# Optimization experiments

Measured on AMD Instinct MI355X. Metric: run time of the kernel, lower is better.

The kernel has to match this reference:

```python
import jax, jax.numpy as jnp
import numpy as np

N_NODES = 100000
N_EDGES = 1250000
HID = 64          # structure_hidden_dim
N_RBF = 32
N_GRAPHS = 512
N_EXPERTS = 8
N_LAYERS = 3
CUTOFF = 6.0
MAX_Z = 100
GATE_IN = HID + N_EXPERTS  # 72
G1, G2 = 64, 32            # gate_hidden_dims


def setup_inputs() -> dict:
    key = jax.random.key(0)
    ks = jax.random.split(key, 32)
    s = 0.05
    inp = {
        'z': jax.random.randint(ks[0], (N_NODES,), 0, MAX_Z),
        'edge_index': jax.random.randint(ks[1], (2, N_EDGES), 0, N_NODES),
        'edge_weight': jax.random.uniform(ks[2], (N_EDGES,), dtype=jnp.float32) * CUTOFF,
        'batch': jnp.sort(jax.random.randint(ks[3], (N_NODES,), 0, N_GRAPHS)),
        'mlip_energies': jax.random.normal(ks[4], (N_GRAPHS, N_EXPERTS), dtype=jnp.float32),
        # SchNet parameters (torch nn.Linear convention: W is [out, in])
        'emb': jax.random.normal(ks[5], (MAX_Z, HID)) * s,
        'fW1': jax.random.normal(ks[6], (N_LAYERS, HID, N_RBF)) * s,
        'fb1': jnp.zeros((N_LAYERS, HID)),
        'fW2': jax.random.normal(ks[7], (N_LAYERS, HID, HID)) * s,
        'fb2': jnp.zeros((N_LAYERS, HID)),
        'dW': jax.random.normal(ks[8], (N_LAYERS, HID, HID)) * s,
        'db': jnp.zeros((N_LAYERS, HID)),
        'uW1': jax.random.normal(ks[9], (N_LAYERS, HID, HID)) * s,
        'ub1': jnp.zeros((N_LAYERS, HID)),
        'uW2': jax.random.normal(ks[10], (N_LAYERS, HID, HID)) * s,
        'ub2': jnp.zeros((N_LAYERS, HID)),
        # Gating MLP: (HID+E) -> 64 -> 32 -> E
        'gW1': jax.random.normal(ks[11], (G1, GATE_IN)) * s,
        'gb1': jnp.zeros((G1,)),
        'gW2': jax.random.normal(ks[12], (G2, G1)) * s,
        'gb2': jnp.zeros((G2,)),
        'gW3': jax.random.normal(ks[13], (N_EXPERTS, G2)) * s,
        'gb3': jnp.zeros((N_EXPERTS,)),
    }
    return inp


def reference(z, edge_index, edge_weight, batch, mlip_energies,
              emb, fW1, fb1, fW2, fb2, dW, db, uW1, ub1, uW2, ub2,
              gW1, gb1, gW2, gb2, gW3, gb3):
    src, dst = edge_index[0], edge_index[1]

    # Gaussian smearing of distances -> [E, N_RBF]
    offsets = jnp.linspace(0.0, CUTOFF, N_RBF, dtype=edge_weight.dtype)
    delta = offsets[1] - offsets[0]
    coeff = -0.5 / (delta * delta)
    diff = edge_weight[:, None] - offsets
    edge_attr = jnp.exp(coeff * diff * diff)

    # atom embedding [N, HID]
    x = emb[z]

    for i in range(N_LAYERS):
        # filter network: Linear -> SiLU -> Linear on RBF features [E, HID]
        f = jax.nn.silu(edge_attr @ fW1[i].T + fb1[i]) @ fW2[i].T + fb2[i]
        # gather + dense + elementwise filter -> messages [E, HID]
        msg = (x[src] @ dW[i].T + db[i]) * f
        # scatter-add to destination nodes [N, HID]
        agg = jax.ops.segment_sum(msg, dst, num_segments=N_NODES)
        # residual update MLP
        x = x + (jax.nn.silu(agg @ uW1[i].T + ub1[i]) @ uW2[i].T + ub2[i])

    # mean pool per graph [G, HID]
    pooled = jax.ops.segment_sum(x, batch, num_segments=N_GRAPHS)
    counts = jax.ops.segment_sum(jnp.ones((N_NODES,), x.dtype), batch, num_segments=N_GRAPHS)
    structure_embedding = pooled / jnp.maximum(counts, 1.0)[:, None]

    # gated MoE head
    gate_in = jnp.concatenate([structure_embedding, mlip_energies], axis=-1)
    h = jax.nn.relu(gate_in @ gW1.T + gb1)
    h = jax.nn.relu(h @ gW2.T + gb2)
    logits = h @ gW3.T + gb3
    weights = jax.nn.softmax(logits, axis=-1)
    prediction = jnp.sum(mlip_energies * weights, axis=-1)
    return (logits, weights, prediction)
```

## Files before the change

kernel.cpp:

```cpp
#include <hip/hip_runtime.h>
#include <hip/hip_fp16.h>
#include <math.h>

#define N_NODES   100000
#define N_EDGES   1250000
#define HID       64
#define N_RBF     32
#define N_GRAPHS  512
#define N_EXPERTS 8
#define N_LAYERS  3
#define CUTOFF    6.0f
#define GATE_IN   72
#define G1_DIM    64
#define G2_DIM    32
#define K_TAB     4096
#define N_BUCKET  391
#define BUCKET_CAP 4608
#define CHUNK_A   8192

typedef short short8 __attribute__((ext_vector_type(8)));
typedef float float4v __attribute__((ext_vector_type(4)));

__device__ __forceinline__ unsigned enc8(float v) {
  unsigned short u = __half_as_ushort(__float2half(v));
  return (unsigned)((unsigned short)(u + 0x80u) >> 8);
}
__device__ __forceinline__ float dec8(unsigned b) {
  return __half2float(__ushort_as_half((unsigned short)(b << 8)));
}
__device__ __forceinline__ unsigned short bf16(float f) {
  unsigned u = __float_as_uint(f);
  u += 0x7fffu + ((u >> 16) & 1u);
  return (unsigned short)(u >> 16);
}

__global__ __launch_bounds__(256) void build_tab(
    const float* __restrict__ fW1, const float* __restrict__ fb1,
    const float* __restrict__ fW2, const float* __restrict__ fb2,
    float* __restrict__ tab) {
  __shared__ float W1s[64][33];
  __shared__ float W2s[64][65];
  __shared__ float rbfs[4][32];
  __shared__ float h1s[4][64];
  int t = threadIdx.x;
  int wv = t >> 6, lane = t & 63;
  int layer = blockIdx.x / 1025;
  int k = (blockIdx.x % 1025) * 4 + wv;

  for (int i = t; i < 64 * 32; i += 256) W1s[i >> 5][i & 31] = fW1[layer * 2048 + i];
  for (int i = t; i < 64 * 64; i += 256) W2s[i >> 6][i & 63] = fW2[layer * 4096 + i];

  float w = (CUTOFF / (float)K_TAB) * (float)k;
  const float delta = CUTOFF / (float)(N_RBF - 1);
  const float coeff = -0.5f / (delta * delta);
  __syncthreads();

  if (lane < N_RBF) {
    float d = w - delta * (float)lane;
    rbfs[wv][lane] = expf(coeff * d * d);
  }
  __syncthreads();

  float s = fb1[layer * HID + lane];
#pragma unroll
  for (int j = 0; j < N_RBF; j++) s += rbfs[wv][j] * W1s[lane][j];
  h1s[wv][lane] = s / (1.0f + expf(-s));
  __syncthreads();

  float f = fb2[layer * HID + lane];
#pragma unroll
  for (int c = 0; c < HID; c++) f += h1s[wv][c] * W2s[lane][c];
  if (k <= K_TAB) tab[(layer * (K_TAB + 1) + k) * HID + lane] = f;
}

__global__ __launch_bounds__(256) void pack_tab8(
    const float* __restrict__ tab, unsigned short* __restrict__ tabP8) {
  int i = blockIdx.x * 256 + threadIdx.x;
  if (i >= N_LAYERS * K_TAB * 64) return;
  int layer = i / (K_TAB * 64);
  int r = i - layer * (K_TAB * 64);
  const float* base = tab + layer * (K_TAB + 1) * 64;
  tabP8[i] = (unsigned short)(enc8(base[r]) | (enc8(base[r + 64]) << 8));
}

__global__ __launch_bounds__(256) void conv_w(
    const float* __restrict__ dW, const float* __restrict__ uW1,
    const float* __restrict__ uW2, unsigned short* __restrict__ dWh,
    unsigned short* __restrict__ uW1h, unsigned short* __restrict__ uW2h) {
  int i = blockIdx.x * 256 + threadIdx.x;
  if (i < N_LAYERS * 4096) {
    dWh[i]  = bf16(dW[i]);
    uW1h[i] = bf16(uW1[i]);
    uW2h[i] = bf16(uW2[i]);
  }
}

__global__ __launch_bounds__(256) void embed_kernel(
    const int* __restrict__ z, const float* __restrict__ emb,
    float* __restrict__ x) {
  int i = blockIdx.x * 256 + threadIdx.x;
  if (i < N_NODES * HID) {
    int n = i >> 6, h = i & 63;
    x[i] = emb[z[n] * HID + h];
  }
}

__global__ __launch_bounds__(256) void partitionA(
    const int* __restrict__ src, const int* __restrict__ dst,
    const float* __restrict__ ew, int* __restrict__ gcnt,
    uint2* __restrict__ stage) {
  __shared__ int hist[N_BUCKET];
  __shared__ int base[N_BUCKET];
  int t = threadIdx.x;
  int e0 = blockIdx.x * CHUNK_A;
  int e1 = e0 + CHUNK_A; if (e1 > N_EDGES) e1 = N_EDGES;

  for (int i = t; i < N_BUCKET; i += 256) hist[i] = 0;
  __syncthreads();
  for (int e = e0 + t; e < e1; e += 256)
    atomicAdd(&hist[dst[e] >> 8], 1);
  __syncthreads();
  for (int i = t; i < N_BUCKET; i += 256) {
    int c = hist[i];
    base[i] = c ? atomicAdd(&gcnt[i], c) : 0;
    hist[i] = 0;
  }
  __syncthreads();
  for (int e = e0 + t; e < e1; e += 256) {
    int d = dst[e];
    int b = d >> 8;
    int r = base[b] + atomicAdd(&hist[b], 1);
    if (r < BUCKET_CAP) {
      float uq = ew[e] * ((float)K_TAB * 8.0f / CUTOFF);
      int wq = (int)(uq + 0.5f);
      if (wq > 32767) wq = 32767;
      stage[(size_t)b * BUCKET_CAP + r] =
          make_uint2(((unsigned)src[e] << 15) | (unsigned)wq, (unsigned)d);
    }
  }
}

__global__ __launch_bounds__(512) void bscan_kernel(
    const int* __restrict__ gcnt, int* __restrict__ bbase,
    int* __restrict__ rowstart) {
  __shared__ int sh[512];
  int t = threadIdx.x;
  int v = 0;
  if (t < N_BUCKET) {
    v = gcnt[t];
    if (v > BUCKET_CAP) v = BUCKET_CAP;
  }
  sh[t] = v;
  __syncthreads();
  for (int off = 1; off < 512; off <<= 1) {
    int add = (t >= off) ? sh[t - off] : 0;
    __syncthreads();
    sh[t] += add;
    __syncthreads();
  }
  if (t < N_BUCKET) bbase[t] = sh[t] - v;
  if (t == N_BUCKET - 1) {
    bbase[N_BUCKET] = sh[t];
    rowstart[N_NODES] = sh[t];
  }
}

__global__ __launch_bounds__(256) void sortB(
    const int* __restrict__ bbase, const uint2* __restrict__ stage,
    int* __restrict__ rowstart, unsigned* __restrict__ recs) {
  __shared__ int cnt[256];
  __shared__ int scn[256];
  __shared__ unsigned dest[BUCKET_CAP];
  int t = threadIdx.x;
  int b = blockIdx.x;
  int node0 = b << 8;
  int base = bbase[b];
  int total = bbase[b + 1] - base;
  const uint2* st = stage + (size_t)b * BUCKET_CAP;

  cnt[t] = 0;
  __syncthreads();
  for (int k = t; k < total; k += 256) atomicAdd(&cnt[(int)st[k].y - node0], 1);
  __syncthreads();
  int v = cnt[t];
  scn[t] = v;
  __syncthreads();
  for (int off = 1; off < 256; off <<= 1) {
    int add = (t >= off) ? scn[t - off] : 0;
    __syncthreads();
    scn[t] += add;
    __syncthreads();
  }
  int excl = scn[t] - v;
  int n = node0 + t;
  if (n < N_NODES) rowstart[n] = base + excl;
  scn[t] = excl;
  cnt[t] = 0;
  __syncthreads();
  for (int k = t; k < total; k += 256) {
    uint2 e = st[k];
    int ln = (int)e.y - node0;
    int r = atomicAdd(&cnt[ln], 1);
    dest[scn[ln] + r] = e.x;
  }
  __syncthreads();
  for (int k = t; k < total; k += 256) recs[base + k] = dest[k];
}

__global__ __launch_bounds__(256, 4) void dense64(
    const float* __restrict__ x, const unsigned short* __restrict__ Wh,
    const float* __restrict__ b, unsigned char* __restrict__ yb) {
  __shared__ __align__(16) unsigned char smem[18432];
  short* As = (short*)smem;
  short* Bs = As + 64 * 72;
  float* Es = (float*)smem;
  int t = threadIdx.x;
  int row0 = blockIdx.x * 64;

#pragma unroll
  for (int it = 0; it < 4; it++) {
    int i = it * 1024 + t * 4;
    int r = i >> 6, c = i & 63;
    int gr = row0 + r;
    float4 v = make_float4(0.f, 0.f, 0.f, 0.f);
    if (gr < N_NODES) v = *(const float4*)&x[(size_t)gr * 64 + c];
    short4 h;
    h.x = (short)bf16(v.x); h.y = (short)bf16(v.y);
    h.z = (short)bf16(v.z); h.w = (short)bf16(v.w);
    *(short4*)&As[r * 72 + c] = h;
  }
#pragma unroll
  for (int it = 0; it < 2; it++) {
    int i = it * 2048 + t * 8;
    int r = i >> 6, c = i & 63;
    *(uint4*)&Bs[r * 72 + c] = *(const uint4*)&Wh[i];
  }
  __syncthreads();

  int lane = t & 63, wv = t >> 6;
  int m = lane & 15, quad = lane >> 4;
  const short* arow = As + (wv * 16 + m) * 72 + quad * 8;
  short8 a0 = *(const short8*)arow;
  short8 a1 = *(const short8*)(arow + 32);
  float4v acc[4];
#pragma unroll
  for (int ct = 0; ct < 4; ct++) {
    const short* brow = Bs + (ct * 16 + m) * 72 + quad * 8;
    short8 bf0 = *(const short8*)brow;
    short8 bf1 = *(const short8*)(brow + 32);
    float bj = b[ct * 16 + m];
    float4v c = {bj, bj, bj, bj};
    c = __builtin_amdgcn_mfma_f32_16x16x32_bf16(a0, bf0, c, 0, 0, 0);
    c = __builtin_amdgcn_mfma_f32_16x16x32_bf16(a1, bf1, c, 0, 0, 0);
    acc[ct] = c;
  }
  __syncthreads();
#pragma unroll
  for (int ct = 0; ct < 4; ct++)
#pragma unroll
    for (int r = 0; r < 4; r++)
      Es[(wv * 16 + quad * 4 + r) * 68 + ct * 16 + m] = acc[ct][r];
  __syncthreads();
  {
    int row = t >> 2, c0 = (t & 3) * 16;
    int gr = row0 + row;
    if (gr < N_NODES) {
      unsigned w[4];
#pragma unroll
      for (int q = 0; q < 4; q++) {
        const float* p = &Es[row * 68 + c0 + 4 * q];
        w[q] = enc8(p[0]) | (enc8(p[1]) << 8) | (enc8(p[2]) << 16) | (enc8(p[3]) << 24);
      }
      *(uint4*)&yb[(size_t)gr * 64 + c0] = make_uint4(w[0], w[1], w[2], w[3]);
    }
  }
}

__global__ __launch_bounds__(256, 4) void update64(
    const unsigned short* __restrict__ aggb,
    const unsigned short* __restrict__ W1h, const float* __restrict__ b1,
    const unsigned short* __restrict__ W2h, const float* __restrict__ b2,
    float* __restrict__ x) {
  __shared__ __align__(16) unsigned char smem[18432];
  short* As = (short*)smem;
  short* Bs = As + 64 * 72;
  float* Es = (float*)smem;
  int t = threadIdx.x;
  int row0 = blockIdx.x * 64;
  int lane = t & 63, wv = t >> 6;
  int m = lane & 15, quad = lane >> 4;

#pragma unroll
  for (int it = 0; it < 2; it++) {
    int i = it * 2048 + t * 8;
    int r = i >> 6, c = i & 63;
    int gr = row0 + r;
    uint4 v = make_uint4(0u, 0u, 0u, 0u);
    if (gr < N_NODES) v = *(const uint4*)&aggb[(size_t)gr * 64 + c];
    *(uint4*)&As[r * 72 + c] = v;
    *(uint4*)&Bs[r * 72 + c] = *(const uint4*)&W1h[i];
  }
  __syncthreads();

  const short* arow = As + (wv * 16 + m) * 72 + quad * 8;
  float4v acc[4];
  {
    short8 a0 = *(const short8*)arow;
    short8 a1 = *(const short8*)(arow + 32);
#pragma unroll
    for (int ct = 0; ct < 4; ct++) {
      const short* brow = Bs + (ct * 16 + m) * 72 + quad * 8;
      short8 bf0 = *(const short8*)brow;
      short8 bf1 = *(const short8*)(brow + 32);
      float bj = b1[ct * 16 + m];
      float4v c = {bj, bj, bj, bj};
      c = __builtin_amdgcn_mfma_f32_16x16x32_bf16(a0, bf0, c, 0, 0, 0);
      c = __builtin_amdgcn_mfma_f32_16x16x32_bf16(a1, bf1, c, 0, 0, 0);
      acc[ct] = c;
    }
  }
  __syncthreads();
#pragma unroll
  for (int ct = 0; ct < 4; ct++)
#pragma unroll
    for (int r = 0; r < 4; r++) {
      float s = acc[ct][r];
      float h = s / (1.0f + expf(-s));
      As[(wv * 16 + quad * 4 + r) * 72 + ct * 16 + m] = (short)bf16(h);
    }
#pragma unroll
  for (int it = 0; it < 2; it++) {
    int i = it * 2048 + t * 8;
    int r = i >> 6, c = i & 63;
    *(uint4*)&Bs[r * 72 + c] = *(const uint4*)&W2h[i];
  }
  __syncthreads();

  {
    short8 a0 = *(const short8*)arow;
    short8 a1 = *(const short8*)(arow + 32);
#pragma unroll
    for (int ct = 0; ct < 4; ct++) {
      const short* brow = Bs + (ct * 16 + m) * 72 + quad * 8;
      short8 bf0 = *(const short8*)brow;
      short8 bf1 = *(const short8*)(brow + 32);
      float bj = b2[ct * 16 + m];
      float4v c = {bj, bj, bj, bj};
      c = __builtin_amdgcn_mfma_f32_16x16x32_bf16(a0, bf0, c, 0, 0, 0);
      c = __builtin_amdgcn_mfma_f32_16x16x32_bf16(a1, bf1, c, 0, 0, 0);
      acc[ct] = c;
    }
  }
  __syncthreads();
#pragma unroll
  for (int ct = 0; ct < 4; ct++)
#pragma unroll
    for (int r = 0; r < 4; r++)
      Es[(wv * 16 + quad * 4 + r) * 68 + ct * 16 + m] = acc[ct][r];
  __syncthreads();
  {
    int row = t >> 2, c0 = (t & 3) * 16;
    int gr = row0 + row;
    if (gr < N_NODES) {
      float* xp = x + (size_t)gr * 64 + c0;
#pragma unroll
      for (int q = 0; q < 4; q++) {
        float4 xv = *(float4*)(xp + 4 * q);
        float4 av = *(const float4*)&Es[row * 68 + c0 + 4 * q];
        xv.x += av.x; xv.y += av.y; xv.z += av.z; xv.w += av.w;
        *(float4*)(xp + 4 * q) = xv;
      }
    }
  }
}

__global__ __launch_bounds__(256) void gather_kernel(
    const int* __restrict__ rowstart, const unsigned* __restrict__ recs,
    const unsigned short* __restrict__ tabP8,
    const unsigned char* __restrict__ yb,
    unsigned short* __restrict__ aggb) {
  int d = blockIdx.x * 4 + (threadIdx.x >> 6);
  int lane = threadIdx.x & 63;
  int b0 = __builtin_amdgcn_readfirstlane(rowstart[d]);
  int b1 = __builtin_amdgcn_readfirstlane(rowstart[d + 1]);
  float acc = 0.0f;
  int j = b0;
  for (; j + 4 <= b1; j += 4) {
    unsigned u0 = recs[j];
    unsigned u1 = recs[j + 1];
    unsigned u2 = recs[j + 2];
    unsigned u3 = recs[j + 3];
    unsigned y0 = yb[((u0 >> 15) << 6) + lane];
    unsigned y1 = yb[((u1 >> 15) << 6) + lane];
    unsigned y2 = yb[((u2 >> 15) << 6) + lane];
    unsigned y3 = yb[((u3 >> 15) << 6) + lane];
    unsigned p0 = tabP8[(((u0 & 32767u) >> 3) << 6) + lane];
    unsigned p1 = tabP8[(((u1 & 32767u) >> 3) << 6) + lane];
    unsigned p2 = tabP8[(((u2 & 32767u) >> 3) << 6) + lane];
    unsigned p3 = tabP8[(((u3 & 32767u) >> 3) << 6) + lane];
    float fr0 = (float)(u0 & 7u) * 0.125f;
    float fr1 = (float)(u1 & 7u) * 0.125f;
    float fr2 = (float)(u2 & 7u) * 0.125f;
    float fr3 = (float)(u3 & 7u) * 0.125f;
    float a0 = dec8(p0 & 0xffu), g0 = dec8(p0 >> 8);
    float a1 = dec8(p1 & 0xffu), g1 = dec8(p1 >> 8);
    float a2 = dec8(p2 & 0xffu), g2 = dec8(p2 >> 8);
    float a3 = dec8(p3 & 0xffu), g3 = dec8(p3 >> 8);
    acc += dec8(y0) * (a0 + (g0 - a0) * fr0);
    acc += dec8(y1) * (a1 + (g1 - a1) * fr1);
    acc += dec8(y2) * (a2 + (g2 - a2) * fr2);
    acc += dec8(y3) * (a3 + (g3 - a3) * fr3);
  }
  for (; j < b1; j++) {
    unsigned u = recs[j];
    unsigned yv = yb[((u >> 15) << 6) + lane];
    unsigned p = tabP8[(((u & 32767u) >> 3) << 6) + lane];
    float fr = (float)(u & 7u) * 0.125f;
    float a = dec8(p & 0xffu), g = dec8(p >> 8);
    acc += dec8(yv) * (a + (g - a) * fr);
  }
  aggb[(size_t)d * 64 + lane] = bf16(acc);
}

__global__ __launch_bounds__(256) void pool_kernel(
    const float* __restrict__ x, const int* __restrict__ batch,
    float* __restrict__ pooled, float* __restrict__ counts) {
  int wid = (blockIdx.x * 256 + threadIdx.x) >> 6;
  int lane = threadIdx.x & 63;
  int n0 = wid * 64;
  if (n0 >= N_NODES) return;
  int n1 = n0 + 64; if (n1 > N_NODES) n1 = N_NODES;
  int curg = batch[n0];
  float acc = 0.0f, cnt = 0.0f;
  for (int n = n0; n < n1; n++) {
    int g = batch[n];
    if (g != curg) {
      unsafeAtomicAdd(&pooled[curg * 64 + lane], acc);
      if (lane == 0) unsafeAtomicAdd(&counts[curg], cnt);
      curg = g; acc = 0.0f; cnt = 0.0f;
    }
    acc += x[n * 64 + lane];
    cnt += 1.0f;
  }
  unsafeAtomicAdd(&pooled[curg * 64 + lane], acc);
  if (lane == 0) unsafeAtomicAdd(&counts[curg], cnt);
}

__global__ __launch_bounds__(256) void gate_kernel(
    const float* __restrict__ pooled, const float* __restrict__ counts,
    const float* __restrict__ mlip,
    const float* __restrict__ gW1, const float* __restrict__ gb1,
    const float* __restrict__ gW2, const float* __restrict__ gb2,
    const float* __restrict__ gW3, const float* __restrict__ gb3,
    float* __restrict__ out) {
  __shared__ float ins[4][GATE_IN];
  __shared__ float h1s[4][G1_DIM];
  __shared__ float h2s[4][G2_DIM];
  __shared__ float lg[4][N_EXPERTS];
  int wv = threadIdx.x >> 6, lane = threadIdx.x & 63;
  int g = blockIdx.x * 4 + wv;

  float cnt = counts[g];
  if (cnt < 1.0f) cnt = 1.0f;
  ins[wv][lane] = pooled[g * 64 + lane] / cnt;
  if (lane < N_EXPERTS) ins[wv][64 + lane] = mlip[g * N_EXPERTS + lane];
  __syncthreads();

  {
    float s = gb1[lane];
    for (int c = 0; c < GATE_IN; c++) s += ins[wv][c] * gW1[lane * GATE_IN + c];
    h1s[wv][lane] = fmaxf(s, 0.0f);
  }
  __syncthreads();
  if (lane < G2_DIM) {
    float s = gb2[lane];
    for (int c = 0; c < G1_DIM; c++) s += h1s[wv][c] * gW2[lane * G1_DIM + c];
    h2s[wv][lane] = fmaxf(s, 0.0f);
  }
  __syncthreads();
  if (lane < N_EXPERTS) {
    float s = gb3[lane];
    for (int c = 0; c < G2_DIM; c++) s += h2s[wv][c] * gW3[lane * G2_DIM + c];
    lg[wv][lane] = s;
  }
  __syncthreads();
  if (lane < N_EXPERTS) {
    float m = -1e30f;
    for (int j = 0; j < N_EXPERTS; j++) m = fmaxf(m, lg[wv][j]);
    float den = 0.0f;
    for (int j = 0; j < N_EXPERTS; j++) den += expf(lg[wv][j] - m);
    float wgt = expf(lg[wv][lane] - m) / den;
    out[g * 8 + lane] = lg[wv][lane];
    out[N_GRAPHS * 8 + g * 8 + lane] = wgt;
    if (lane == 0) {
      float p = 0.0f;
      for (int j = 0; j < N_EXPERTS; j++)
        p += mlip[g * 8 + j] * expf(lg[wv][j] - m) / den;
      out[N_GRAPHS * 16 + g] = p;
    }
  }
}

extern "C" void kernel_launch(void* const* d_in, const int* in_sizes, int n_in,
                              void* d_out, int out_size, void* d_ws, size_t ws_size,
                              hipStream_t stream) {
  const int*   z     = (const int*)  d_in[0];
  const int*   ei    = (const int*)  d_in[1];
  const float* ew    = (const float*)d_in[2];
  const int*   batch = (const int*)  d_in[3];
  const float* mlip  = (const float*)d_in[4];
  const float* emb   = (const float*)d_in[5];
  const float* fW1   = (const float*)d_in[6];
  const float* fb1   = (const float*)d_in[7];
  const float* fW2   = (const float*)d_in[8];
  const float* fb2   = (const float*)d_in[9];
  const float* dW    = (const float*)d_in[10];
  const float* db    = (const float*)d_in[11];
  const float* uW1   = (const float*)d_in[12];
  const float* ub1   = (const float*)d_in[13];
  const float* uW2   = (const float*)d_in[14];
  const float* ub2   = (const float*)d_in[15];
  const float* gW1   = (const float*)d_in[16];
  const float* gb1   = (const float*)d_in[17];
  const float* gW2   = (const float*)d_in[18];
  const float* gb2   = (const float*)d_in[19];
  const float* gW3   = (const float*)d_in[20];
  const float* gb3   = (const float*)d_in[21];

  const int* src = ei;
  const int* dst = ei + N_EDGES;

  float* ws = (float*)d_ws;
  float*          x        = ws;
  unsigned char*  yb       = (unsigned char*)(ws + 6400000);
  unsigned short* aggb     = (unsigned short*)(ws + 8000000);
  float*          tab      = ws + 11200000;
  unsigned short* tabP8    = (unsigned short*)(ws + 11986624);
  float*          pooled   = ws + 12379840;
  float*          counts   = ws + 12412608;
  int*            rowstart = (int*)(ws + 12413120);
  unsigned*       recs     = (unsigned*)(ws + 12513121);
  int*            gcnt     = (int*)(ws + 13763121);
  int*            bbase    = (int*)(ws + 13763512);
  uint2*          stage    = (uint2*)(ws + 13763904);
  unsigned short* dWh      = (unsigned short*)(ws + 17367360);
  unsigned short* uW1h     = dWh + N_LAYERS * 4096;
  unsigned short* uW2h     = uW1h + N_LAYERS * 4096;

  hipMemsetAsync(gcnt, 0, N_BUCKET * sizeof(int), stream);
  partitionA<<<(N_EDGES + CHUNK_A - 1) / CHUNK_A, 256, 0, stream>>>(
      src, dst, ew, gcnt, stage);
  bscan_kernel<<<1, 512, 0, stream>>>(gcnt, bbase, rowstart);
  sortB<<<N_BUCKET, 256, 0, stream>>>(bbase, stage, rowstart, recs);

  build_tab<<<N_LAYERS * 1025, 256, 0, stream>>>(fW1, fb1, fW2, fb2, tab);
  pack_tab8<<<(N_LAYERS * K_TAB * 64) / 256, 256, 0, stream>>>(tab, tabP8);
  conv_w<<<(N_LAYERS * 4096 + 255) / 256, 256, 0, stream>>>(dW, uW1, uW2, dWh, uW1h, uW2h);
  embed_kernel<<<(N_NODES * HID + 255) / 256, 256, 0, stream>>>(z, emb, x);

  for (int i = 0; i < N_LAYERS; i++) {
    dense64<<<(N_NODES + 63) / 64, 256, 0, stream>>>(x, dWh + i * 4096, db + i * 64, yb);
    gather_kernel<<<(N_NODES + 3) / 4, 256, 0, stream>>>(
        rowstart, recs, tabP8 + i * K_TAB * 64, yb, aggb);
    update64<<<(N_NODES + 63) / 64, 256, 0, stream>>>(aggb, uW1h + i * 4096, ub1 + i * 64,
                                                      uW2h + i * 4096, ub2 + i * 64, x);
  }

  hipMemsetAsync(pooled, 0, (size_t)(N_GRAPHS * HID + N_GRAPHS) * sizeof(float), stream);
  pool_kernel<<<(N_NODES / 64 + 1 + 3) / 4, 256, 0, stream>>>(x, batch, pooled, counts);
  gate_kernel<<<N_GRAPHS / 4, 256, 0, stream>>>(pooled, counts, mlip,
                                                gW1, gb1, gW2, gb2, gW3, gb3,
                                                (float*)d_out);
}
```

Before: 419.4 us.

## Fuse update with next-layer dense, drop embed kernel, single-byte filter table

The residual update kernel now also runs the next layer's dense projection and writes the quantized messages. The first layer reads embeddings straight from z/emb, so the separate embed kernel and a full read-modify-write of x go away. The filter table becomes one byte per entry, taken as the midpoint of adjacent bins instead of an interpolated pair, which halves table traffic in the gather and removes the interpolation arithmetic but loses accuracy. The change also shrinks the partition chunk size and gives the sort kernel 512 threads.

```diff
diff --git a/kernel.cpp b/kernel.cpp
--- a/kernel.cpp
+++ b/kernel.cpp
@@ -16,7 +16,7 @@
 #define K_TAB     4096
 #define N_BUCKET  391
 #define BUCKET_CAP 4608
-#define CHUNK_A   8192
+#define CHUNK_A   2048
 
 typedef short short8 __attribute__((ext_vector_type(8)));
 typedef float float4v __attribute__((ext_vector_type(4)));
@@ -74,13 +74,13 @@
 }
 
 __global__ __launch_bounds__(256) void pack_tab8(
-    const float* __restrict__ tab, unsigned short* __restrict__ tabP8) {
+    const float* __restrict__ tab, unsigned char* __restrict__ tab8) {
   int i = blockIdx.x * 256 + threadIdx.x;
   if (i >= N_LAYERS * K_TAB * 64) return;
   int layer = i / (K_TAB * 64);
   int r = i - layer * (K_TAB * 64);
   const float* base = tab + layer * (K_TAB + 1) * 64;
-  tabP8[i] = (unsigned short)(enc8(base[r]) | (enc8(base[r + 64]) << 8));
+  tab8[i] = (unsigned char)enc8(0.5f * (base[r] + base[r + 64]));
 }
 
 __global__ __launch_bounds__(256) void conv_w(
@@ -95,16 +95,6 @@
   }
 }
 
-__global__ __launch_bounds__(256) void embed_kernel(
-    const int* __restrict__ z, const float* __restrict__ emb,
-    float* __restrict__ x) {
-  int i = blockIdx.x * 256 + threadIdx.x;
-  if (i < N_NODES * HID) {
-    int n = i >> 6, h = i & 63;
-    x[i] = emb[z[n] * HID + h];
-  }
-}
-
 __global__ __launch_bounds__(256) void partitionA(
     const int* __restrict__ src, const int* __restrict__ dst,
     const float* __restrict__ ew, int* __restrict__ gcnt,
@@ -131,11 +121,11 @@
     int b = d >> 8;
     int r = base[b] + atomicAdd(&hist[b], 1);
     if (r < BUCKET_CAP) {
-      float uq = ew[e] * ((float)K_TAB * 8.0f / CUTOFF);
-      int wq = (int)(uq + 0.5f);
-      if (wq > 32767) wq = 32767;
+      float uq = ew[e] * ((float)K_TAB / CUTOFF);
+      int wq = (int)uq;
+      if (wq > K_TAB - 1) wq = K_TAB - 1;
       stage[(size_t)b * BUCKET_CAP + r] =
-          make_uint2(((unsigned)src[e] << 15) | (unsigned)wq, (unsigned)d);
+          make_uint2(((unsigned)src[e] << 12) | (unsigned)wq, (unsigned)d);
     }
   }
 }
@@ -165,7 +155,7 @@
   }
 }
 
-__global__ __launch_bounds__(256) void sortB(
+__global__ __launch_bounds__(512) void sortB(
     const int* __restrict__ bbase, const uint2* __restrict__ stage,
     int* __restrict__ rowstart, unsigned* __restrict__ recs) {
   __shared__ int cnt[256];
@@ -178,37 +168,40 @@
   int total = bbase[b + 1] - base;
   const uint2* st = stage + (size_t)b * BUCKET_CAP;
 
-  cnt[t] = 0;
-  __syncthreads();
-  for (int k = t; k < total; k += 256) atomicAdd(&cnt[(int)st[k].y - node0], 1);
-  __syncthreads();
-  int v = cnt[t];
-  scn[t] = v;
+  if (t < 256) cnt[t] = 0;
+  __syncthreads();
+  for (int k = t; k < total; k += 512) atomicAdd(&cnt[(int)st[k].y - node0], 1);
+  __syncthreads();
+  int v = 0;
+  if (t < 256) { v = cnt[t]; scn[t] = v; }
   __syncthreads();
   for (int off = 1; off < 256; off <<= 1) {
-    int add = (t >= off) ? scn[t - off] : 0;
+    int add = (t < 256 && t >= off) ? scn[t - off] : 0;
     __syncthreads();
-    scn[t] += add;
+    if (t < 256) scn[t] += add;
     __syncthreads();
   }
-  int excl = scn[t] - v;
-  int n = node0 + t;
-  if (n < N_NODES) rowstart[n] = base + excl;
-  scn[t] = excl;
-  cnt[t] = 0;
-  __syncthreads();
-  for (int k = t; k < total; k += 256) {
+  if (t < 256) {
+    int excl = scn[t] - v;
+    int n = node0 + t;
+    if (n < N_NODES) rowstart[n] = base + excl;
+    scn[t] = excl;
+    cnt[t] = 0;
+  }
+  __syncthreads();
+  for (int k = t; k < total; k += 512) {
     uint2 e = st[k];
     int ln = (int)e.y - node0;
     int r = atomicAdd(&cnt[ln], 1);
     dest[scn[ln] + r] = e.x;
   }
   __syncthreads();
-  for (int k = t; k < total; k += 256) recs[base + k] = dest[k];
-}
-
-__global__ __launch_bounds__(256, 4) void dense64(
-    const float* __restrict__ x, const unsigned short* __restrict__ Wh,
+  for (int k = t; k < total; k += 512) recs[base + k] = dest[k];
+}
+
+__global__ __launch_bounds__(256, 4) void dense0(
+    const int* __restrict__ z, const float* __restrict__ emb,
+    const unsigned short* __restrict__ Wh,
     const float* __restrict__ b, unsigned char* __restrict__ yb) {
   __shared__ __align__(16) unsigned char smem[18432];
   short* As = (short*)smem;
@@ -223,7 +216,10 @@
     int r = i >> 6, c = i & 63;
     int gr = row0 + r;
     float4 v = make_float4(0.f, 0.f, 0.f, 0.f);
-    if (gr < N_NODES) v = *(const float4*)&x[(size_t)gr * 64 + c];
+    if (gr < N_NODES) {
+      int zi = z[gr];
+      v = *(const float4*)&emb[(size_t)zi * 64 + c];
+    }
     short4 h;
     h.x = (short)bf16(v.x); h.y = (short)bf16(v.y);
     h.z = (short)bf16(v.z); h.w = (short)bf16(v.w);
@@ -276,20 +272,38 @@
   }
 }
 
-__global__ __launch_bounds__(256, 4) void update64(
+__global__ __launch_bounds__(256, 4) void update_dense(
     const unsigned short* __restrict__ aggb,
-    const unsigned short* __restrict__ W1h, const float* __restrict__ b1,
-    const unsigned short* __restrict__ W2h, const float* __restrict__ b2,
-    float* __restrict__ x) {
-  __shared__ __align__(16) unsigned char smem[18432];
-  short* As = (short*)smem;
-  short* Bs = As + 64 * 72;
-  float* Es = (float*)smem;
+    const unsigned short* __restrict__ W1h, const float* __restrict__ ub1,
+    const unsigned short* __restrict__ W2h, const float* __restrict__ ub2,
+    float* __restrict__ x,
+    const int* __restrict__ z, const float* __restrict__ emb,
+    const unsigned short* __restrict__ dWn, const float* __restrict__ dbn,
+    unsigned char* __restrict__ yb) {
+  __shared__ __align__(16) short A1[64 * 72];
+  __shared__ __align__(16) short B1[64 * 72];
+  __shared__ __align__(16) float E[64 * 68];
   int t = threadIdx.x;
   int row0 = blockIdx.x * 64;
   int lane = t & 63, wv = t >> 6;
   int m = lane & 15, quad = lane >> 4;
 
+#pragma unroll
+  for (int it = 0; it < 4; it++) {
+    int i = it * 1024 + t * 4;
+    int r = i >> 6, c = i & 63;
+    int gr = row0 + r;
+    float4 v = make_float4(0.f, 0.f, 0.f, 0.f);
+    if (gr < N_NODES) {
+      if (z) {
+        int zi = z[gr];
+        v = *(const float4*)&emb[(size_t)zi * 64 + c];
+      } else {
+        v = *(const float4*)&x[(size_t)gr * 64 + c];
+      }
+    }
+    *(float4*)&E[r * 68 + c] = v;
+  }
 #pragma unroll
   for (int it = 0; it < 2; it++) {
     int i = it * 2048 + t * 8;
@@ -297,22 +311,22 @@
     int gr = row0 + r;
     uint4 v = make_uint4(0u, 0u, 0u, 0u);
     if (gr < N_NODES) v = *(const uint4*)&aggb[(size_t)gr * 64 + c];
-    *(uint4*)&As[r * 72 + c] = v;
-    *(uint4*)&Bs[r * 72 + c] = *(const uint4*)&W1h[i];
-  }
-  __syncthreads();
-
-  const short* arow = As + (wv * 16 + m) * 72 + quad * 8;
+    *(uint4*)&A1[r * 72 + c] = v;
+    *(uint4*)&B1[r * 72 + c] = *(const uint4*)&W1h[i];
+  }
+  __syncthreads();
+
+  const short* arow = A1 + (wv * 16 + m) * 72 + quad * 8;
   float4v acc[4];
   {
     short8 a0 = *(const short8*)arow;
     short8 a1 = *(const short8*)(arow + 32);
 #pragma unroll
     for (int ct = 0; ct < 4; ct++) {
-      const short* brow = Bs + (ct * 16 + m) * 72 + quad * 8;
+      const short* brow = B1 + (ct * 16 + m) * 72 + quad * 8;
       short8 bf0 = *(const short8*)brow;
       short8 bf1 = *(const short8*)(brow + 32);
-      float bj = b1[ct * 16 + m];
+      float bj = ub1[ct * 16 + m];
       float4v c = {bj, bj, bj, bj};
       c = __builtin_amdgcn_mfma_f32_16x16x32_bf16(a0, bf0, c, 0, 0, 0);
       c = __builtin_amdgcn_mfma_f32_16x16x32_bf16(a1, bf1, c, 0, 0, 0);
@@ -326,13 +340,13 @@
     for (int r = 0; r < 4; r++) {
       float s = acc[ct][r];
       float h = s / (1.0f + expf(-s));
-      As[(wv * 16 + quad * 4 + r) * 72 + ct * 16 + m] = (short)bf16(h);
+      A1[(wv * 16 + quad * 4 + r) * 72 + ct * 16 + m] = (short)bf16(h);
     }
 #pragma unroll
   for (int it = 0; it < 2; it++) {
     int i = it * 2048 + t * 8;
     int r = i >> 6, c = i & 63;
-    *(uint4*)&Bs[r * 72 + c] = *(const uint4*)&W2h[i];
+    *(uint4*)&B1[r * 72 + c] = *(const uint4*)&W2h[i];
   }
   __syncthreads();
 
@@ -341,10 +355,10 @@
     short8 a1 = *(const short8*)(arow + 32);
 #pragma unroll
     for (int ct = 0; ct < 4; ct++) {
-      const short* brow = Bs + (ct * 16 + m) * 72 + quad * 8;
+      const short* brow = B1 + (ct * 16 + m) * 72 + quad * 8;
       short8 bf0 = *(const short8*)brow;
       short8 bf1 = *(const short8*)(brow + 32);
-      float bj = b2[ct * 16 + m];
+      float bj = ub2[ct * 16 + m];
       float4v c = {bj, bj, bj, bj};
       c = __builtin_amdgcn_mfma_f32_16x16x32_bf16(a0, bf0, c, 0, 0, 0);
       c = __builtin_amdgcn_mfma_f32_16x16x32_bf16(a1, bf1, c, 0, 0, 0);
@@ -356,7 +370,7 @@
   for (int ct = 0; ct < 4; ct++)
 #pragma unroll
     for (int r = 0; r < 4; r++)
-      Es[(wv * 16 + quad * 4 + r) * 68 + ct * 16 + m] = acc[ct][r];
+      E[(wv * 16 + quad * 4 + r) * 68 + ct * 16 + m] += acc[ct][r];
   __syncthreads();
   {
     int row = t >> 2, c0 = (t & 3) * 16;
@@ -364,19 +378,69 @@
     if (gr < N_NODES) {
       float* xp = x + (size_t)gr * 64 + c0;
 #pragma unroll
+      for (int q = 0; q < 4; q++)
+        *(float4*)(xp + 4 * q) = *(const float4*)&E[row * 68 + c0 + 4 * q];
+    }
+  }
+  if (!dWn) return;
+
+#pragma unroll
+  for (int it = 0; it < 4; it++) {
+    int i = it * 1024 + t * 4;
+    int r = i >> 6, c = i & 63;
+    float4 v = *(const float4*)&E[r * 68 + c];
+    short4 h;
+    h.x = (short)bf16(v.x); h.y = (short)bf16(v.y);
+    h.z = (short)bf16(v.z); h.w = (short)bf16(v.w);
+    *(short4*)&A1[r * 72 + c] = h;
+  }
+#pragma unroll
+  for (int it = 0; it < 2; it++) {
+    int i = it * 2048 + t * 8;
+    int r = i >> 6, c = i & 63;
+    *(uint4*)&B1[r * 72 + c] = *(const uint4*)&dWn[i];
+  }
+  __syncthreads();
+  {
+    short8 a0 = *(const short8*)arow;
+    short8 a1 = *(const short8*)(arow + 32);
+#pragma unroll
+    for (int ct = 0; ct < 4; ct++) {
+      const short* brow = B1 + (ct * 16 + m) * 72 + quad * 8;
+      short8 bf0 = *(const short8*)brow;
+      short8 bf1 = *(const short8*)(brow + 32);
+      float bj = dbn[ct * 16 + m];
+      float4v c = {bj, bj, bj, bj};
+      c = __builtin_amdgcn_mfma_f32_16x16x32_bf16(a0, bf0, c, 0, 0, 0);
+      c = __builtin_amdgcn_mfma_f32_16x16x32_bf16(a1, bf1, c, 0, 0, 0);
+      acc[ct] = c;
+    }
+  }
+  __syncthreads();
+#pragma unroll
+  for (int ct = 0; ct < 4; ct++)
+#pragma unroll
+    for (int r = 0; r < 4; r++)
+      E[(wv * 16 + quad * 4 + r) * 68 + ct * 16 + m] = acc[ct][r];
+  __syncthreads();
+  {
+    int row = t >> 2, c0 = (t & 3) * 16;
+    int gr = row0 + row;
+    if (gr < N_NODES) {
+      unsigned w[4];
+#pragma unroll
       for (int q = 0; q < 4; q++) {
-        float4 xv = *(float4*)(xp + 4 * q);
-        float4 av = *(const float4*)&Es[row * 68 + c0 + 4 * q];
-        xv.x += av.x; xv.y += av.y; xv.z += av.z; xv.w += av.w;
-        *(float4*)(xp + 4 * q) = xv;
+        const float* p = &E[row * 68 + c0 + 4 * q];
+        w[q] = enc8(p[0]) | (enc8(p[1]) << 8) | (enc8(p[2]) << 16) | (enc8(p[3]) << 24);
       }
+      *(uint4*)&yb[(size_t)gr * 64 + c0] = make_uint4(w[0], w[1], w[2], w[3]);
     }
   }
 }
 
 __global__ __launch_bounds__(256) void gather_kernel(
     const int* __restrict__ rowstart, const unsigned* __restrict__ recs,
-    const unsigned short* __restrict__ tabP8,
+    const unsigned char* __restrict__ tab8,
     const unsigned char* __restrict__ yb,
     unsigned short* __restrict__ aggb) {
   int d = blockIdx.x * 4 + (threadIdx.x >> 6);
@@ -390,34 +454,24 @@
     unsigned u1 = recs[j + 1];
     unsigned u2 = recs[j + 2];
     unsigned u3 = recs[j + 3];
-    unsigned y0 = yb[((u0 >> 15) << 6) + lane];
-    unsigned y1 = yb[((u1 >> 15) << 6) + lane];
-    unsigned y2 = yb[((u2 >> 15) << 6) + lane];
-    unsigned y3 = yb[((u3 >> 15) << 6) + lane];
-    unsigned p0 = tabP8[(((u0 & 32767u) >> 3) << 6) + lane];
-    unsigned p1 = tabP8[(((u1 & 32767u) >> 3) << 6) + lane];
-    unsigned p2 = tabP8[(((u2 & 32767u) >> 3) << 6) + lane];
-    unsigned p3 = tabP8[(((u3 & 32767u) >> 3) << 6) + lane];
-    float fr0 = (float)(u0 & 7u) * 0.125f;
-    float fr1 = (float)(u1 & 7u) * 0.125f;
-    float fr2 = (float)(u2 & 7u) * 0.125f;
-    float fr3 = (float)(u3 & 7u) * 0.125f;
-    float a0 = dec8(p0 & 0xffu), g0 = dec8(p0 >> 8);
-    float a1 = dec8(p1 & 0xffu), g1 = dec8(p1 >> 8);
-    float a2 = dec8(p2 & 0xffu), g2 = dec8(p2 >> 8);
-    float a3 = dec8(p3 & 0xffu), g3 = dec8(p3 >> 8);
-    acc += dec8(y0) * (a0 + (g0 - a0) * fr0);
-    acc += dec8(y1) * (a1 + (g1 - a1) * fr1);
-    acc += dec8(y2) * (a2 + (g2 - a2) * fr2);
-    acc += dec8(y3) * (a3 + (g3 - a3) * fr3);
+    unsigned y0 = yb[((u0 >> 12) << 6) + lane];
+    unsigned y1 = yb[((u1 >> 12) << 6) + lane];
+    unsigned y2 = yb[((u2 >> 12) << 6) + lane];
+    unsigned y3 = yb[((u3 >> 12) << 6) + lane];
+    unsigned f0 = tab8[((u0 & 4095u) << 6) + lane];
+    unsigned f1 = tab8[((u1 & 4095u) << 6) + lane];
+    unsigned f2 = tab8[((u2 & 4095u) << 6) + lane];
+    unsigned f3 = tab8[((u3 & 4095u) << 6) + lane];
+    acc += dec8(y0) * dec8(f0);
+    acc += dec8(y1) * dec8(f1);
+    acc += dec8(y2) * dec8(f2);
+    acc += dec8(y3) * dec8(f3);
   }
   for (; j < b1; j++) {
     unsigned u = recs[j];
-    unsigned yv = yb[((u >> 15) << 6) + lane];
-    unsigned p = tabP8[(((u & 32767u) >> 3) << 6) + lane];
-    float fr = (float)(u & 7u) * 0.125f;
-    float a = dec8(p & 0xffu), g = dec8(p >> 8);
-    acc += dec8(yv) * (a + (g - a) * fr);
+    unsigned yv = yb[((u >> 12) << 6) + lane];
+    unsigned fv = tab8[((u & 4095u) << 6) + lane];
+    acc += dec8(yv) * dec8(fv);
   }
   aggb[(size_t)d * 64 + lane] = bf16(acc);
 }
@@ -535,15 +589,15 @@
   unsigned char*  yb       = (unsigned char*)(ws + 6400000);
   unsigned short* aggb     = (unsigned short*)(ws + 8000000);
   float*          tab      = ws + 11200000;
-  unsigned short* tabP8    = (unsigned short*)(ws + 11986624);
-  float*          pooled   = ws + 12379840;
-  float*          counts   = ws + 12412608;
-  int*            rowstart = (int*)(ws + 12413120);
-  unsigned*       recs     = (unsigned*)(ws + 12513121);
-  int*            gcnt     = (int*)(ws + 13763121);
-  int*            bbase    = (int*)(ws + 13763512);
-  uint2*          stage    = (uint2*)(ws + 13763904);
-  unsigned short* dWh      = (unsigned short*)(ws + 17367360);
+  unsigned char*  tab8     = (unsigned char*)(ws + 11986624);
+  float*          pooled   = ws + 12183232;
+  float*          counts   = ws + 12216000;
+  int*            rowstart = (int*)(ws + 12216512);
+  unsigned*       recs     = (unsigned*)(ws + 12316513);
+  int*            gcnt     = (int*)(ws + 13566513);
+  int*            bbase    = (int*)(ws + 13566904);
+  uint2*          stage    = (uint2*)(ws + 13567296);
+  unsigned short* dWh      = (unsigned short*)(ws + 17171008);
   unsigned short* uW1h     = dWh + N_LAYERS * 4096;
   unsigned short* uW2h     = uW1h + N_LAYERS * 4096;
 
@@ -551,20 +605,24 @@
   partitionA<<<(N_EDGES + CHUNK_A - 1) / CHUNK_A, 256, 0, stream>>>(
       src, dst, ew, gcnt, stage);
   bscan_kernel<<<1, 512, 0, stream>>>(gcnt, bbase, rowstart);
-  sortB<<<N_BUCKET, 256, 0, stream>>>(bbase, stage, rowstart, recs);
+  sortB<<<N_BUCKET, 512, 0, stream>>>(bbase, stage, rowstart, recs);
 
   build_tab<<<N_LAYERS * 1025, 256, 0, stream>>>(fW1, fb1, fW2, fb2, tab);
-  pack_tab8<<<(N_LAYERS * K_TAB * 64) / 256, 256, 0, stream>>>(tab, tabP8);
+  pack_tab8<<<(N_LAYERS * K_TAB * 64) / 256, 256, 0, stream>>>(tab, tab8);
   conv_w<<<(N_LAYERS * 4096 + 255) / 256, 256, 0, stream>>>(dW, uW1, uW2, dWh, uW1h, uW2h);
-  embed_kernel<<<(N_NODES * HID + 255) / 256, 256, 0, stream>>>(z, emb, x);
-
-  for (int i = 0; i < N_LAYERS; i++) {
-    dense64<<<(N_NODES + 63) / 64, 256, 0, stream>>>(x, dWh + i * 4096, db + i * 64, yb);
-    gather_kernel<<<(N_NODES + 3) / 4, 256, 0, stream>>>(
-        rowstart, recs, tabP8 + i * K_TAB * 64, yb, aggb);
-    update64<<<(N_NODES + 63) / 64, 256, 0, stream>>>(aggb, uW1h + i * 4096, ub1 + i * 64,
-                                                      uW2h + i * 4096, ub2 + i * 64, x);
-  }
+
+  const int NBLK = (N_NODES + 63) / 64;
+  dense0<<<NBLK, 256, 0, stream>>>(z, emb, dWh, db, yb);
+
+  gather_kernel<<<N_NODES / 4, 256, 0, stream>>>(rowstart, recs, tab8, yb, aggb);
+  update_dense<<<NBLK, 256, 0, stream>>>(aggb, uW1h, ub1, uW2h, ub2, x,
+                                         z, emb, dWh + 4096, db + 64, yb);
+  gather_kernel<<<N_NODES / 4, 256, 0, stream>>>(rowstart, recs, tab8 + K_TAB * 64, yb, aggb);
+  update_dense<<<NBLK, 256, 0, stream>>>(aggb, uW1h + 4096, ub1 + 64, uW2h + 4096, ub2 + 64, x,
+                                         nullptr, nullptr, dWh + 8192, db + 128, yb);
+  gather_kernel<<<N_NODES / 4, 256, 0, stream>>>(rowstart, recs, tab8 + 2 * K_TAB * 64, yb, aggb);
+  update_dense<<<NBLK, 256, 0, stream>>>(aggb, uW1h + 8192, ub1 + 128, uW2h + 8192, ub2 + 128, x,
+                                         nullptr, nullptr, nullptr, nullptr, nullptr);
 
   hipMemsetAsync(pooled, 0, (size_t)(N_GRAPHS * HID + N_GRAPHS) * sizeof(float), stream);
   pool_kernel<<<(N_NODES / 64 + 1 + 3) / 4, 256, 0, stream>>>(x, batch, pooled, counts);
```

Result: faster. 395.3 us (-5.7%).
